# Performance work log

Measured on AMD Instinct MI355X. Metric: run time of the kernel, lower is better.

The kernel has to match this reference:

```python
import jax, jax.numpy as jnp
import numpy as np

BATCH, NBITS = 32768, 512


def setup_inputs() -> dict:
    key = jax.random.key(0)
    raw = jax.random.randint(key, (BATCH, NBITS), 0, 2)
    bits = raw.astype(jnp.float32) * 2.0 - 1.0  # values in {-1, +1}
    return {"bits": bits}


def _joint_prob(b):
    # b in {0,1}, shape [B, N]. p_ij[i,j,m,n] = mean_b 1[b_i==m] * 1[b_j==n]
    B = b.shape[0]
    ind = jnp.stack([(b == 0.0), (b == 1.0)], axis=0).astype(b.dtype)  # [2, B, N]
    return jnp.einsum('mbi,nbj->ijmn', ind, ind) / B  # [N, N, 2, 2]


def reference(bits):
    b = bits / 2.0 + 0.5
    N = b.shape[1]
    p_ij = _joint_prob(b)
    p_i_pos = b.mean(axis=0)
    p_i = jnp.stack([1.0 - p_i_pos, p_i_pos], axis=-1)  # [N, 2]
    outer = p_i[:, None, :, None] * p_i[None, :, None, :]  # [N, N, 2, 2]
    ii = jnp.arange(N)
    tri = (ii[:, None] > ii[None, :])[:, :, None, None]  # triangle: keep i > j
    valid = tri & (p_ij > 0) & (p_i[:, None, :, None] > 0) & (p_i[None, :, None, :] > 0)
    safe_p = jnp.where(valid, p_ij, 1.0)
    safe_o = jnp.where(valid, outer, 1.0)
    terms = jnp.where(valid, safe_p * jnp.log(safe_p / safe_o), 0.0)
    cnt = valid.sum().astype(bits.dtype)
    return terms.sum() / cnt
```

## Files before the change

### kernel.cpp

```cpp
#include <hip/hip_runtime.h>
#include <stdint.h>

#define BATCH   32768
#define NBITS   512
#define NWORDS  512
#define NSLICE  16
#define SW      32
#define NT32    136
#define MIGRID  512

typedef unsigned long long u64;

__global__ __launch_bounds__(256) void pack_kernel(const float* __restrict__ bits,
                                                   u64* __restrict__ packed,
                                                   double* __restrict__ lg,
                                                   int* __restrict__ c1,
                                                   int* __restrict__ done) {
    const int gid = blockIdx.x * 256 + threadIdx.x;

    if (gid <= BATCH) lg[gid] = (gid > 0) ? log((double)gid) : 0.0;
    if (gid < NBITS) c1[gid] = 0;
    if (gid == NBITS) *done = 0;

    const int wv   = threadIdx.x >> 6;
    const int lane = threadIdx.x & 63;
    const int gw   = blockIdx.x * 4 + wv;
    const int w    = gw >> 2;
    const int q    = gw & 3;
    const int c0   = q * 128 + lane * 2;

    u64 m0 = 0, m1 = 0;
    const float* base = bits + (size_t)w * 64 * NBITS + c0;
#pragma unroll 16
    for (int r = 0; r < 64; ++r) {
        float2 v = *reinterpret_cast<const float2*>(base + (size_t)r * NBITS);
        const u64 b = 1ull << r;
        if (v.x > 0.0f) m0 |= b;
        if (v.y > 0.0f) m1 |= b;
    }
    ulonglong2 st; st.x = m0; st.y = m1;
    *reinterpret_cast<ulonglong2*>(&packed[(size_t)w * NBITS + c0]) = st;
}

__global__ __launch_bounds__(64) void gram_kernel(const u64* __restrict__ packed,
                                                  int* __restrict__ Cp,
                                                  int* __restrict__ c1) {
    __shared__ u64 ldsI[SW][32];
    __shared__ u64 ldsJ[SW][32];

    const int s = blockIdx.x & (NSLICE - 1);
    const int t = blockIdx.x >> 4;
    int bi = (int)((sqrtf(8.0f * (float)t + 1.0f) - 1.0f) * 0.5f);
    while ((bi + 1) * (bi + 2) / 2 <= t) ++bi;
    while (bi * (bi + 1) / 2 > t) --bi;
    const int bj = t - bi * (bi + 1) / 2;

    const int i0 = bi * 32, j0 = bj * 32;
    const int w0 = s * SW;
    const bool diag = (bi == bj);

    for (int q = threadIdx.x; q < SW * 16; q += 64) {
        const int wo = q >> 4, cp = (q & 15) * 2;
        const size_t g = (size_t)(w0 + wo) * NBITS;
        *reinterpret_cast<ulonglong2*>(&ldsI[wo][cp]) =
            *reinterpret_cast<const ulonglong2*>(&packed[g + i0 + cp]);
        if (!diag)
            *reinterpret_cast<ulonglong2*>(&ldsJ[wo][cp]) =
                *reinterpret_cast<const ulonglong2*>(&packed[g + j0 + cp]);
    }
    __syncthreads();

    const int tx4 = (threadIdx.x & 7) * 4;
    const int ty4 = (threadIdx.x >> 3) * 4;
    const u64 (*BJ)[32] = diag ? ldsI : ldsJ;

    int acc[4][4] = {};
#pragma unroll 4
    for (int w = 0; w < SW; ++w) {
        const u64 a0 = ldsI[w][ty4],     a1 = ldsI[w][ty4 + 1];
        const u64 a2 = ldsI[w][ty4 + 2], a3 = ldsI[w][ty4 + 3];
        const u64 b0 = BJ[w][tx4],       b1 = BJ[w][tx4 + 1];
        const u64 b2 = BJ[w][tx4 + 2],   b3 = BJ[w][tx4 + 3];
        acc[0][0] += __popcll(a0 & b0); acc[0][1] += __popcll(a0 & b1);
        acc[0][2] += __popcll(a0 & b2); acc[0][3] += __popcll(a0 & b3);
        acc[1][0] += __popcll(a1 & b0); acc[1][1] += __popcll(a1 & b1);
        acc[1][2] += __popcll(a1 & b2); acc[1][3] += __popcll(a1 & b3);
        acc[2][0] += __popcll(a2 & b0); acc[2][1] += __popcll(a2 & b1);
        acc[2][2] += __popcll(a2 & b2); acc[2][3] += __popcll(a2 & b3);
        acc[3][0] += __popcll(a3 & b0); acc[3][1] += __popcll(a3 & b1);
        acc[3][2] += __popcll(a3 & b2); acc[3][3] += __popcll(a3 & b3);
    }

    int* out = Cp + (size_t)s * NBITS * NBITS;
#pragma unroll
    for (int a = 0; a < 4; ++a)
        *reinterpret_cast<int4*>(&out[(size_t)(i0 + ty4 + a) * NBITS + j0 + tx4]) =
            make_int4(acc[a][0], acc[a][1], acc[a][2], acc[a][3]);

    if (diag && tx4 == ty4) {
#pragma unroll
        for (int a = 0; a < 4; ++a)
            atomicAdd(&c1[i0 + ty4 + a], acc[a][a]);
    }
}

__global__ __launch_bounds__(256) void mi_kernel(const int* __restrict__ Cp,
                                                 const int* __restrict__ c1,
                                                 const double* __restrict__ lg,
                                                 double* __restrict__ bsum,
                                                 int* __restrict__ bcnt,
                                                 int* __restrict__ done,
                                                 float* __restrict__ out) {
    const double invB = 1.0 / (double)BATCH;
    const int i = blockIdx.x;
    const int ci = c1[i];
    const double lgB = lg[BATCH];
    double lsum = 0.0;
    int lcnt = 0;

#pragma unroll
    for (int half = 0; half < 2; ++half) {
        const int j = half * 256 + threadIdx.x;
        if (j < i) {
            int n11 = 0;
#pragma unroll
            for (int s = 0; s < NSLICE; ++s)
                n11 += Cp[(size_t)s * NBITS * NBITS + (size_t)i * NBITS + j];
            const int cj = c1[j];

            const int pim[2] = {BATCH - ci, ci};
            const int pjn[2] = {BATCH - cj, cj};
            const int nmn[2][2] = {{BATCH - ci - cj + n11, cj - n11},
                                   {ci - n11, n11}};
#pragma unroll
            for (int m = 0; m < 2; ++m)
#pragma unroll
                for (int n = 0; n < 2; ++n) {
                    const int c_mn = nmn[m][n];
                    if (c_mn > 0 && pim[m] > 0 && pjn[n] > 0) {
                        lsum += (double)c_mn * invB *
                                (lg[c_mn] + lgB - lg[pim[m]] - lg[pjn[n]]);
                        ++lcnt;
                    }
                }
        }
    }

    __shared__ double ssum[256];
    __shared__ int scnt[256];
    __shared__ int lastFlag;
    ssum[threadIdx.x] = lsum;
    scnt[threadIdx.x] = lcnt;
    __syncthreads();
    for (int off = 128; off > 0; off >>= 1) {
        if (threadIdx.x < off) {
            ssum[threadIdx.x] += ssum[threadIdx.x + off];
            scnt[threadIdx.x] += scnt[threadIdx.x + off];
        }
        __syncthreads();
    }
    if (threadIdx.x == 0) {
        bsum[i] = ssum[0];
        bcnt[i] = scnt[0];
        __threadfence();
        lastFlag = (atomicAdd(done, 1) == MIGRID - 1);
    }
    __syncthreads();
    if (!lastFlag) return;

    __threadfence();
    double s2 = bsum[threadIdx.x] + bsum[threadIdx.x + 256];
    int c2 = bcnt[threadIdx.x] + bcnt[threadIdx.x + 256];
    __syncthreads();
    ssum[threadIdx.x] = s2;
    scnt[threadIdx.x] = c2;
    __syncthreads();
    for (int off = 128; off > 0; off >>= 1) {
        if (threadIdx.x < off) {
            ssum[threadIdx.x] += ssum[threadIdx.x + off];
            scnt[threadIdx.x] += scnt[threadIdx.x + off];
        }
        __syncthreads();
    }
    if (threadIdx.x == 0) out[0] = (float)(ssum[0] / (double)scnt[0]);
}

extern "C" void kernel_launch(void* const* d_in, const int* in_sizes, int n_in,
                              void* d_out, int out_size, void* d_ws, size_t ws_size,
                              hipStream_t stream) {
    const float* bits = (const float*)d_in[0];
    char* ws = (char*)d_ws;
    u64*    packed = (u64*)ws;
    int*    Cp     = (int*)(ws + (2u << 20));
    double* lg     = (double*)(ws + (18u << 20));
    int*    c1     = (int*)(ws + (18u << 20) + (512u << 10));
    int*    done   = (int*)(ws + (18u << 20) + (516u << 10));
    double* bsum   = (double*)(ws + (18u << 20) + (576u << 10));
    int*    bcnt   = (int*)(ws + (18u << 20) + (640u << 10));

    pack_kernel<<<512, 256, 0, stream>>>(bits, packed, lg, c1, done);
    gram_kernel<<<NT32 * NSLICE, 64, 0, stream>>>(packed, Cp, c1);
    mi_kernel<<<MIGRID, 256, 0, stream>>>(Cp, c1, lg, bsum, bcnt, done, (float*)d_out);
}
```

Before: 50.60 us.

## Split gram into more batch slices and pack four tile tasks per block

Doubles the number of batch slices (32 slices of 16 words each) so the popcount Gram work spreads over more wavefronts, and groups four independent tile tasks per 256-thread block with per-wave shared memory. The intent is higher occupancy and less per-block launch overhead in the Gram stage. The cost is twice as many partial-sum matrices written to memory and read back by mi_kernel (which now loops over 32 slices), and the workspace layout moves to fit the larger buffer.

```diff
diff --git a/kernel.cpp b/kernel.cpp
--- a/kernel.cpp
+++ b/kernel.cpp
@@ -4,9 +4,10 @@
 #define BATCH   32768
 #define NBITS   512
 #define NWORDS  512
-#define NSLICE  16
-#define SW      32
+#define NSLICE  32
+#define SW      16
 #define NT32    136
+#define GBLK    1088
 #define MIGRID  512
 
 typedef unsigned long long u64;
@@ -42,14 +43,17 @@
     *reinterpret_cast<ulonglong2*>(&packed[(size_t)w * NBITS + c0]) = st;
 }
 
-__global__ __launch_bounds__(64) void gram_kernel(const u64* __restrict__ packed,
-                                                  int* __restrict__ Cp,
-                                                  int* __restrict__ c1) {
-    __shared__ u64 ldsI[SW][32];
-    __shared__ u64 ldsJ[SW][32];
-
-    const int s = blockIdx.x & (NSLICE - 1);
-    const int t = blockIdx.x >> 4;
+__global__ __launch_bounds__(256) void gram_kernel(const u64* __restrict__ packed,
+                                                   int* __restrict__ Cp,
+                                                   int* __restrict__ c1) {
+    __shared__ u64 lds[4][2][SW][32];
+
+    const int wid  = threadIdx.x >> 6;
+    const int lane = threadIdx.x & 63;
+    const int task = blockIdx.x * 4 + wid;
+    const int s = task & (NSLICE - 1);
+    const int t = task >> 5;
+
     int bi = (int)((sqrtf(8.0f * (float)t + 1.0f) - 1.0f) * 0.5f);
     while ((bi + 1) * (bi + 2) / 2 <= t) ++bi;
     while (bi * (bi + 1) / 2 > t) --bi;
@@ -59,28 +63,29 @@
     const int w0 = s * SW;
     const bool diag = (bi == bj);
 
-    for (int q = threadIdx.x; q < SW * 16; q += 64) {
+    for (int q = lane; q < SW * 16; q += 64) {
         const int wo = q >> 4, cp = (q & 15) * 2;
         const size_t g = (size_t)(w0 + wo) * NBITS;
-        *reinterpret_cast<ulonglong2*>(&ldsI[wo][cp]) =
+        *reinterpret_cast<ulonglong2*>(&lds[wid][0][wo][cp]) =
             *reinterpret_cast<const ulonglong2*>(&packed[g + i0 + cp]);
         if (!diag)
-            *reinterpret_cast<ulonglong2*>(&ldsJ[wo][cp]) =
+            *reinterpret_cast<ulonglong2*>(&lds[wid][1][wo][cp]) =
                 *reinterpret_cast<const ulonglong2*>(&packed[g + j0 + cp]);
     }
     __syncthreads();
 
-    const int tx4 = (threadIdx.x & 7) * 4;
-    const int ty4 = (threadIdx.x >> 3) * 4;
-    const u64 (*BJ)[32] = diag ? ldsI : ldsJ;
+    const int tx4 = (lane & 7) * 4;
+    const int ty4 = (lane >> 3) * 4;
+    const u64 (*LI)[32] = lds[wid][0];
+    const u64 (*LJ)[32] = diag ? lds[wid][0] : lds[wid][1];
 
     int acc[4][4] = {};
 #pragma unroll 4
     for (int w = 0; w < SW; ++w) {
-        const u64 a0 = ldsI[w][ty4],     a1 = ldsI[w][ty4 + 1];
-        const u64 a2 = ldsI[w][ty4 + 2], a3 = ldsI[w][ty4 + 3];
-        const u64 b0 = BJ[w][tx4],       b1 = BJ[w][tx4 + 1];
-        const u64 b2 = BJ[w][tx4 + 2],   b3 = BJ[w][tx4 + 3];
+        const u64 a0 = LI[w][ty4],     a1 = LI[w][ty4 + 1];
+        const u64 a2 = LI[w][ty4 + 2], a3 = LI[w][ty4 + 3];
+        const u64 b0 = LJ[w][tx4],     b1 = LJ[w][tx4 + 1];
+        const u64 b2 = LJ[w][tx4 + 2], b3 = LJ[w][tx4 + 3];
         acc[0][0] += __popcll(a0 & b0); acc[0][1] += __popcll(a0 & b1);
         acc[0][2] += __popcll(a0 & b2); acc[0][3] += __popcll(a0 & b3);
         acc[1][0] += __popcll(a1 & b0); acc[1][1] += __popcll(a1 & b1);
@@ -192,13 +197,13 @@
     char* ws = (char*)d_ws;
     u64*    packed = (u64*)ws;
     int*    Cp     = (int*)(ws + (2u << 20));
-    double* lg     = (double*)(ws + (18u << 20));
-    int*    c1     = (int*)(ws + (18u << 20) + (512u << 10));
-    int*    done   = (int*)(ws + (18u << 20) + (516u << 10));
-    double* bsum   = (double*)(ws + (18u << 20) + (576u << 10));
-    int*    bcnt   = (int*)(ws + (18u << 20) + (640u << 10));
+    double* lg     = (double*)(ws + (34u << 20));
+    int*    c1     = (int*)(ws + (34u << 20) + (512u << 10));
+    int*    done   = (int*)(ws + (34u << 20) + (516u << 10));
+    double* bsum   = (double*)(ws + (34u << 20) + (576u << 10));
+    int*    bcnt   = (int*)(ws + (34u << 20) + (640u << 10));
 
     pack_kernel<<<512, 256, 0, stream>>>(bits, packed, lg, c1, done);
-    gram_kernel<<<NT32 * NSLICE, 64, 0, stream>>>(packed, Cp, c1);
+    gram_kernel<<<GBLK, 256, 0, stream>>>(packed, Cp, c1);
     mi_kernel<<<MIGRID, 256, 0, stream>>>(Cp, c1, lg, bsum, bcnt, done, (float*)d_out);
 }
```

New measurement: 54.31 us. 7.3% more time.
